# Performance work log

Measured on AMD Instinct MI355X. Metric: run time of the kernel, lower is better.

## Reference

```python
import jax, jax.numpy as jnp
import numpy as np
import itertools

# ---- model dimensions ----
NELEC = 10   # total electrons
NSPIN = 2    # spin_split = 2 -> equal split (5, 5)
NPER = 5     # electrons per spin block
D = 3        # spatial dimension
NION = 2     # number of ions (diatomic)
DP = 32      # backflow output feature dim d'
NDENSE = 64  # ndense_resnet


def _perms_and_signs(n):
    perms = np.array(list(itertools.permutations(range(n))), dtype=np.int32)
    signs = np.empty(len(perms), dtype=np.float32)
    for i, p in enumerate(perms):
        inv = sum(1 for a in range(n) for b in range(a + 1, n) if p[a] > p[b])
        signs[i] = -1.0 if inv % 2 else 1.0
    return jnp.asarray(perms), jnp.asarray(signs)

# constant permutation indices/signs (closed over; not differentiated)
PERMS, SIGNS = _perms_and_signs(NPER)  # (120, 5), (120,)


def setup_inputs() -> dict:
    key = jax.random.key(0)
    ks = jax.random.split(key, 8)
    B = 2048
    feat = NION * D + NION  # backflow input features per electron: r_ei flat + |r_ei|
    nin = NPER * DP         # flattened spin-block input to each ResNet
    return {
        "elec_pos": jax.random.normal(ks[0], (B, NELEC, D), jnp.float32),
        "ion_pos": jax.random.normal(ks[1], (NION, D), jnp.float32) * 2.0,
        "bf_w": jax.random.normal(ks[2], (feat, DP), jnp.float32) / np.sqrt(feat),
        "bf_b": jnp.zeros((DP,), jnp.float32),
        "w0": jax.random.normal(ks[3], (NSPIN, nin, NDENSE), jnp.float32) / np.sqrt(nin),
        "b0": jnp.zeros((NSPIN, NDENSE), jnp.float32),
        "w1": jax.random.normal(ks[4], (NSPIN, NDENSE, NDENSE), jnp.float32) / np.sqrt(NDENSE),
        "b1": jnp.zeros((NSPIN, NDENSE), jnp.float32),
        "w2": jax.random.normal(ks[5], (NSPIN, NDENSE, 1), jnp.float32) / np.sqrt(NDENSE),
        "b2": jnp.zeros((NSPIN, 1), jnp.float32),
        "jastrow_kernel": jnp.ones((NION,), jnp.float32),
    }


def _spin_antisym(block, W0, B0, W1, B1, W2, B2):
    # block: (B, NPER, DP) one spin block of the 1e stream
    B = block.shape[0]
    xp = block[:, PERMS, :]                  # (B, nperm, NPER, DP) all permutations
    xp = xp.reshape(B, PERMS.shape[0], NPER * DP)
    # SimpleResNet: dense->act, residual middle layer, final linear to 1
    h = jnp.tanh(xp @ W0 + B0)
    h = jnp.tanh(h @ W1 + B1) + h            # residual (shapes match)
    out = (h @ W2 + B2)[..., 0]              # (B, nperm)
    return jnp.sum(out * SIGNS, axis=-1)     # signed perm-sum -> (B,)


def reference(elec_pos, ion_pos, bf_w, bf_b, w0, b0, w1, b1, w2, b2, jastrow_kernel):
    B = elec_pos.shape[0]
    # backflow: r_ei features -> dense -> tanh
    r_ei = elec_pos[..., :, None, :] - ion_pos          # (B, nelec, nion, d)
    r_norm = jnp.linalg.norm(r_ei, axis=-1)             # (B, nelec, nion)
    feats = jnp.concatenate([r_ei.reshape(B, NELEC, NION * D), r_norm], axis=-1)
    stream_1e = jnp.tanh(feats @ bf_w + bf_b)           # (B, nelec, DP)
    # split into equal spin blocks (spin_split=2)
    blocks = jnp.stack(jnp.split(stream_1e, NSPIN, axis=-2), axis=0)  # (NSPIN, B, NPER, DP)
    per_spin = jax.vmap(_spin_antisym)(blocks, w0, b0, w1, b1, w2, b2)  # (NSPIN, B)
    antisymmetric_part = jnp.log(jnp.abs(jnp.prod(per_spin, axis=0)))   # (B,)
    # isotropic atomic exponential decay jastrow (log domain)
    jastrow_part = -jnp.sum(jastrow_kernel * r_norm, axis=(-1, -2))     # (B,)
    return antisymmetric_part + jastrow_part
```

## Files before the change

### kernel.cpp

```cpp
#include <hip/hip_runtime.h>
#include <math.h>

#define NELEC 10
#define NSPIN 2
#define NPER 5
#define DIM 3
#define NION 2
#define DP 32
#define NDENSE 64
#define NPERM 120
#define RS 324
#define HTS 124

__device__ __forceinline__ float fast_tanh(float x) {
    float e = __expf(2.0f * x);
    return 1.0f - 2.0f * __builtin_amdgcn_rcpf(e + 1.0f);
}

__device__ __forceinline__ unsigned pick_remove(unsigned& el, int d) {
    unsigned v = (el >> (4 * d)) & 0xFu;
    unsigned low = el & ((1u << (4 * d)) - 1u);
    el = low | ((el >> (4 * (d + 1))) << (4 * d));
    return v;
}

__global__ __launch_bounds__(128, 1) void antisym_kern(
    const float* __restrict__ elec_pos, const float* __restrict__ ion_pos,
    const float* __restrict__ bf_w, const float* __restrict__ bf_b,
    const float* __restrict__ w0, const float* __restrict__ b0,
    const float* __restrict__ w1, const float* __restrict__ b1,
    const float* __restrict__ w2,
    float* __restrict__ psum, int B)
{
    const int b = blockIdx.x;
    const int s = blockIdx.y;
    const int t = threadIdx.x;
    const int wave = t >> 6, lane = t & 63;

    __shared__ float s1e[NPER * DP];
    __shared__ __align__(16) float G[NPER][RS];
    __shared__ __align__(16) float HT[NDENSE][HTS];
    __shared__ double red[4];

    const float* ep = elec_pos + (b * NELEC + s * NPER) * DIM;
    const float i0x = ion_pos[0], i0y = ion_pos[1], i0z = ion_pos[2];
    const float i1x = ion_pos[3], i1y = ion_pos[4], i1z = ion_pos[5];
    for (int idx = t; idx < NPER * DP; idx += 128) {
        int j = idx >> 5, c = idx & 31;
        float ex = ep[j * 3 + 0], ey = ep[j * 3 + 1], ez = ep[j * 3 + 2];
        float dx0 = ex - i0x, dy0 = ey - i0y, dz0 = ez - i0z;
        float dx1 = ex - i1x, dy1 = ey - i1y, dz1 = ez - i1z;
        float n0 = sqrtf(dx0 * dx0 + dy0 * dy0 + dz0 * dz0);
        float n1 = sqrtf(dx1 * dx1 + dy1 * dy1 + dz1 * dz1);
        float acc = bf_b[c];
        acc += dx0 * bf_w[0 * DP + c];
        acc += dy0 * bf_w[1 * DP + c];
        acc += dz0 * bf_w[2 * DP + c];
        acc += dx1 * bf_w[3 * DP + c];
        acc += dy1 * bf_w[4 * DP + c];
        acc += dz1 * bf_w[5 * DP + c];
        acc += n0 * bf_w[6 * DP + c];
        acc += n1 * bf_w[7 * DP + c];
        s1e[idx] = fast_tanh(acc);
    }
    __syncthreads();

    const float* w0s = w0 + s * (NPER * DP) * NDENSE;
    for (int j = wave; j < NPER; j += 2) {
        float4 sv4[8];
        #pragma unroll
        for (int q = 0; q < 8; q++) sv4[q] = *(const float4*)(s1e + j * DP + q * 4);
        #pragma unroll
        for (int i = 0; i < NPER; i++) {
            float acc = 0.f;
            #pragma unroll
            for (int q = 0; q < 8; q++) {
                const float* wb = w0s + (i * DP + q * 4) * NDENSE + lane;
                acc += sv4[q].x * wb[0 * NDENSE];
                acc += sv4[q].y * wb[1 * NDENSE];
                acc += sv4[q].z * wb[2 * NDENSE];
                acc += sv4[q].w * wb[3 * NDENSE];
            }
            G[j][i * NDENSE + lane] = acc;
        }
    }
    __syncthreads();

    const int pid = wave * 60 + lane;
    float sign = 0.f;
    int p0 = 0, p1 = 0, p2 = 0, p3 = 0, p4 = 0;
    if (lane < 60) {
        int p = pid;
        unsigned el = 0x43210u;
        int d0 = p / 24; p -= d0 * 24;
        int d1 = p / 6;  p -= d1 * 6;
        int d2 = p / 2;  p -= d2 * 2;
        int d3 = p;
        p0 = pick_remove(el, d0);
        p1 = pick_remove(el, d1);
        p2 = pick_remove(el, d2);
        p3 = pick_remove(el, d3);
        p4 = el & 0xF;
        sign = ((d0 + d1 + d2 + d3) & 1) ? -1.f : 1.f;
    }

    const float* b0s = b0 + s * NDENSE;
    const float* w2s = w2 + s * NDENSE;
    const float* g0 = &G[p0][0 * NDENSE];
    const float* g1 = &G[p1][1 * NDENSE];
    const float* g2 = &G[p2][2 * NDENSE];
    const float* g3 = &G[p3][3 * NDENSE];
    const float* g4 = &G[p4][4 * NDENSE];

    float hdot = 0.f;
    #pragma unroll
    for (int cc = 0; cc < NDENSE / 4; cc++) {
        float4 a = *(const float4*)(b0s + cc * 4);
        float4 q;
        q = *(const float4*)(g0 + cc * 4); a.x += q.x; a.y += q.y; a.z += q.z; a.w += q.w;
        q = *(const float4*)(g1 + cc * 4); a.x += q.x; a.y += q.y; a.z += q.z; a.w += q.w;
        q = *(const float4*)(g2 + cc * 4); a.x += q.x; a.y += q.y; a.z += q.z; a.w += q.w;
        q = *(const float4*)(g3 + cc * 4); a.x += q.x; a.y += q.y; a.z += q.z; a.w += q.w;
        q = *(const float4*)(g4 + cc * 4); a.x += q.x; a.y += q.y; a.z += q.z; a.w += q.w;
        float t0 = fast_tanh(a.x), t1 = fast_tanh(a.y), t2 = fast_tanh(a.z), t3 = fast_tanh(a.w);
        if (lane < 60) {
            HT[cc * 4 + 0][pid] = t0;
            HT[cc * 4 + 1][pid] = t1;
            HT[cc * 4 + 2][pid] = t2;
            HT[cc * 4 + 3][pid] = t3;
        }
        hdot += t0 * w2s[cc * 4 + 0] + t1 * w2s[cc * 4 + 1]
              + t2 * w2s[cc * 4 + 2] + t3 * w2s[cc * 4 + 3];
    }

    double dvh = (double)(sign * hdot);
    #pragma unroll
    for (int off = 32; off > 0; off >>= 1) dvh += __shfl_down(dvh, off, 64);
    if (lane == 0) red[wave] = dvh;
    __syncthreads();

    const int pg = lane >> 3, jg = lane & 7;
    const int pb = wave ? (56 + 8 * pg) : (8 * pg);
    const float* w1s = w1 + s * NDENSE * NDENSE;
    const float* b1s = b1 + s * NDENSE;
    const float* wgp = w1s + 8 * jg;

    float v[8][8];
    #pragma unroll
    for (int i = 0; i < 8; i++)
        #pragma unroll
        for (int r = 0; r < 8; r++) v[i][r] = 0.f;

    #pragma unroll 4
    for (int k = 0; k < NDENSE; k++) {
        float4 ha = *(const float4*)(&HT[k][pb]);
        float4 hb = *(const float4*)(&HT[k][pb + 4]);
        float4 wa = *(const float4*)(wgp + k * NDENSE);
        float4 wb = *(const float4*)(wgp + k * NDENSE + 4);
        float hv[8] = {ha.x, ha.y, ha.z, ha.w, hb.x, hb.y, hb.z, hb.w};
        float wv[8] = {wa.x, wa.y, wa.z, wa.w, wb.x, wb.y, wb.z, wb.w};
        #pragma unroll
        for (int i = 0; i < 8; i++)
            #pragma unroll
            for (int r = 0; r < 8; r++)
                v[i][r] = fmaf(hv[i], wv[r], v[i][r]);
    }

    float4 b1a = *(const float4*)(b1s + 8 * jg);
    float4 b1b = *(const float4*)(b1s + 8 * jg + 4);
    float4 w2a = *(const float4*)(w2s + 8 * jg);
    float4 w2b = *(const float4*)(w2s + 8 * jg + 4);
    const float b1v[8] = {b1a.x, b1a.y, b1a.z, b1a.w, b1b.x, b1b.y, b1b.z, b1b.w};
    const float w2v[8] = {w2a.x, w2a.y, w2a.z, w2a.w, w2b.x, w2b.y, w2b.z, w2b.w};

    float lanesum = 0.f;
    #pragma unroll
    for (int i = 0; i < 8; i++) {
        int p = pb + i;
        int d0 = p / 24;  int r0 = p - 24 * d0;
        int d1 = r0 / 6;  int r1 = r0 - 6 * d1;
        int d2 = r1 >> 1; int d3 = r1 & 1;
        float sgn = ((d0 + d1 + d2 + d3) & 1) ? -1.f : 1.f;
        if (wave == 1 && pg == 0) sgn = 0.f;
        float si = 0.f;
        #pragma unroll
        for (int r = 0; r < 8; r++)
            si = fmaf(fast_tanh(v[i][r] + b1v[r]), w2v[r], si);
        lanesum = fmaf(sgn, si, lanesum);
    }

    double dvj = (double)lanesum;
    #pragma unroll
    for (int off = 32; off > 0; off >>= 1) dvj += __shfl_down(dvj, off, 64);
    if (lane == 0) red[2 + wave] = dvj;
    __syncthreads();
    if (t == 0) psum[s * B + b] = (float)((red[0] + red[1]) + (red[2] + red[3]));
}

__global__ void combine_kern(const float* __restrict__ psum,
                             const float* __restrict__ elec_pos,
                             const float* __restrict__ ion_pos,
                             const float* __restrict__ jk,
                             float* __restrict__ out, int B)
{
    int b = blockIdx.x * 256 + threadIdx.x;
    if (b >= B) return;
    const float i0x = ion_pos[0], i0y = ion_pos[1], i0z = ion_pos[2];
    const float i1x = ion_pos[3], i1y = ion_pos[4], i1z = ion_pos[5];
    const float j0 = jk[0], j1 = jk[1];
    const float* ep = elec_pos + b * NELEC * DIM;
    float jas = 0.f;
    #pragma unroll
    for (int e = 0; e < NELEC; e++) {
        float ex = ep[e * 3 + 0], ey = ep[e * 3 + 1], ez = ep[e * 3 + 2];
        float dx0 = ex - i0x, dy0 = ey - i0y, dz0 = ez - i0z;
        float dx1 = ex - i1x, dy1 = ey - i1y, dz1 = ez - i1z;
        jas += j0 * sqrtf(dx0 * dx0 + dy0 * dy0 + dz0 * dz0);
        jas += j1 * sqrtf(dx1 * dx1 + dy1 * dy1 + dz1 * dz1);
    }
    float ps0 = psum[b], ps1 = psum[B + b];
    out[b] = logf(fabsf(ps0 * ps1)) - jas;
}

extern "C" void kernel_launch(void* const* d_in, const int* in_sizes, int n_in,
                              void* d_out, int out_size, void* d_ws, size_t ws_size,
                              hipStream_t stream) {
    const float* elec_pos = (const float*)d_in[0];
    const float* ion_pos  = (const float*)d_in[1];
    const float* bf_w     = (const float*)d_in[2];
    const float* bf_b     = (const float*)d_in[3];
    const float* w0       = (const float*)d_in[4];
    const float* b0       = (const float*)d_in[5];
    const float* w1       = (const float*)d_in[6];
    const float* b1       = (const float*)d_in[7];
    const float* w2       = (const float*)d_in[8];
    const float* jk       = (const float*)d_in[10];
    float* out = (float*)d_out;

    const int B = in_sizes[0] / (NELEC * DIM);

    float* psum = (float*)d_ws;

    hipLaunchKernelGGL(antisym_kern,
                       dim3(B, NSPIN), dim3(128), 0, stream,
                       elec_pos, ion_pos, bf_w, bf_b, w0, b0, w1, b1, w2, psum, B);
    hipLaunchKernelGGL(combine_kern,
                       dim3((B + 255) / 256), dim3(256), 0, stream,
                       psum, elec_pos, ion_pos, jk, out, B);
}
```

Before: 165.2 us.

## Double block size to 256 threads and split dense layer work finer

```diff
diff --git a/kernel.cpp b/kernel.cpp
--- a/kernel.cpp
+++ b/kernel.cpp
@@ -24,7 +24,7 @@
     return v;
 }
 
-__global__ __launch_bounds__(128, 1) void antisym_kern(
+__global__ __launch_bounds__(256, 1) void antisym_kern(
     const float* __restrict__ elec_pos, const float* __restrict__ ion_pos,
     const float* __restrict__ bf_w, const float* __restrict__ bf_b,
     const float* __restrict__ w0, const float* __restrict__ b0,
@@ -40,12 +40,13 @@
     __shared__ float s1e[NPER * DP];
     __shared__ __align__(16) float G[NPER][RS];
     __shared__ __align__(16) float HT[NDENSE][HTS];
-    __shared__ double red[4];
+    __shared__ double red_h[2];
+    __shared__ double red_j[4];
 
     const float* ep = elec_pos + (b * NELEC + s * NPER) * DIM;
     const float i0x = ion_pos[0], i0y = ion_pos[1], i0z = ion_pos[2];
     const float i1x = ion_pos[3], i1y = ion_pos[4], i1z = ion_pos[5];
-    for (int idx = t; idx < NPER * DP; idx += 128) {
+    for (int idx = t; idx < NPER * DP; idx += 256) {
         int j = idx >> 5, c = idx & 31;
         float ex = ep[j * 3 + 0], ey = ep[j * 3 + 1], ez = ep[j * 3 + 2];
         float dx0 = ex - i0x, dy0 = ey - i0y, dz0 = ez - i0z;
@@ -66,7 +67,7 @@
     __syncthreads();
 
     const float* w0s = w0 + s * (NPER * DP) * NDENSE;
-    for (int j = wave; j < NPER; j += 2) {
+    for (int j = wave; j < NPER; j += 4) {
         float4 sv4[8];
         #pragma unroll
         for (int q = 0; q < 8; q++) sv4[q] = *(const float4*)(s1e + j * DP + q * 4);
@@ -86,81 +87,82 @@
     }
     __syncthreads();
 
-    const int pid = wave * 60 + lane;
-    float sign = 0.f;
-    int p0 = 0, p1 = 0, p2 = 0, p3 = 0, p4 = 0;
-    if (lane < 60) {
-        int p = pid;
-        unsigned el = 0x43210u;
-        int d0 = p / 24; p -= d0 * 24;
-        int d1 = p / 6;  p -= d1 * 6;
-        int d2 = p / 2;  p -= d2 * 2;
-        int d3 = p;
-        p0 = pick_remove(el, d0);
-        p1 = pick_remove(el, d1);
-        p2 = pick_remove(el, d2);
-        p3 = pick_remove(el, d3);
-        p4 = el & 0xF;
-        sign = ((d0 + d1 + d2 + d3) & 1) ? -1.f : 1.f;
-    }
-
     const float* b0s = b0 + s * NDENSE;
     const float* w2s = w2 + s * NDENSE;
-    const float* g0 = &G[p0][0 * NDENSE];
-    const float* g1 = &G[p1][1 * NDENSE];
-    const float* g2 = &G[p2][2 * NDENSE];
-    const float* g3 = &G[p3][3 * NDENSE];
-    const float* g4 = &G[p4][4 * NDENSE];
-
-    float hdot = 0.f;
-    #pragma unroll
-    for (int cc = 0; cc < NDENSE / 4; cc++) {
-        float4 a = *(const float4*)(b0s + cc * 4);
-        float4 q;
-        q = *(const float4*)(g0 + cc * 4); a.x += q.x; a.y += q.y; a.z += q.z; a.w += q.w;
-        q = *(const float4*)(g1 + cc * 4); a.x += q.x; a.y += q.y; a.z += q.z; a.w += q.w;
-        q = *(const float4*)(g2 + cc * 4); a.x += q.x; a.y += q.y; a.z += q.z; a.w += q.w;
-        q = *(const float4*)(g3 + cc * 4); a.x += q.x; a.y += q.y; a.z += q.z; a.w += q.w;
-        q = *(const float4*)(g4 + cc * 4); a.x += q.x; a.y += q.y; a.z += q.z; a.w += q.w;
-        float t0 = fast_tanh(a.x), t1 = fast_tanh(a.y), t2 = fast_tanh(a.z), t3 = fast_tanh(a.w);
-        if (lane < 60) {
-            HT[cc * 4 + 0][pid] = t0;
-            HT[cc * 4 + 1][pid] = t1;
-            HT[cc * 4 + 2][pid] = t2;
-            HT[cc * 4 + 3][pid] = t3;
+
+    if (wave < 2) {
+        float sign = 0.f;
+        int p0 = 0, p1 = 0, p2 = 0, p3 = 0, p4 = 0;
+        if (t < NPERM) {
+            int p = t;
+            unsigned el = 0x43210u;
+            int d0 = p / 24; p -= d0 * 24;
+            int d1 = p / 6;  p -= d1 * 6;
+            int d2 = p / 2;  p -= d2 * 2;
+            int d3 = p;
+            p0 = pick_remove(el, d0);
+            p1 = pick_remove(el, d1);
+            p2 = pick_remove(el, d2);
+            p3 = pick_remove(el, d3);
+            p4 = el & 0xF;
+            sign = ((d0 + d1 + d2 + d3) & 1) ? -1.f : 1.f;
         }
-        hdot += t0 * w2s[cc * 4 + 0] + t1 * w2s[cc * 4 + 1]
-              + t2 * w2s[cc * 4 + 2] + t3 * w2s[cc * 4 + 3];
-    }
-
-    double dvh = (double)(sign * hdot);
-    #pragma unroll
-    for (int off = 32; off > 0; off >>= 1) dvh += __shfl_down(dvh, off, 64);
-    if (lane == 0) red[wave] = dvh;
-    __syncthreads();
-
-    const int pg = lane >> 3, jg = lane & 7;
-    const int pb = wave ? (56 + 8 * pg) : (8 * pg);
+        const float* g0 = &G[p0][0 * NDENSE];
+        const float* g1 = &G[p1][1 * NDENSE];
+        const float* g2 = &G[p2][2 * NDENSE];
+        const float* g3 = &G[p3][3 * NDENSE];
+        const float* g4 = &G[p4][4 * NDENSE];
+
+        float hdot = 0.f;
+        #pragma unroll
+        for (int cc = 0; cc < NDENSE / 4; cc++) {
+            float4 a = *(const float4*)(b0s + cc * 4);
+            float4 q;
+            q = *(const float4*)(g0 + cc * 4); a.x += q.x; a.y += q.y; a.z += q.z; a.w += q.w;
+            q = *(const float4*)(g1 + cc * 4); a.x += q.x; a.y += q.y; a.z += q.z; a.w += q.w;
+            q = *(const float4*)(g2 + cc * 4); a.x += q.x; a.y += q.y; a.z += q.z; a.w += q.w;
+            q = *(const float4*)(g3 + cc * 4); a.x += q.x; a.y += q.y; a.z += q.z; a.w += q.w;
+            q = *(const float4*)(g4 + cc * 4); a.x += q.x; a.y += q.y; a.z += q.z; a.w += q.w;
+            float t0 = fast_tanh(a.x), t1 = fast_tanh(a.y), t2 = fast_tanh(a.z), t3 = fast_tanh(a.w);
+            if (t < NPERM) {
+                HT[cc * 4 + 0][t] = t0;
+                HT[cc * 4 + 1][t] = t1;
+                HT[cc * 4 + 2][t] = t2;
+                HT[cc * 4 + 3][t] = t3;
+            }
+            hdot += t0 * w2s[cc * 4 + 0] + t1 * w2s[cc * 4 + 1]
+                  + t2 * w2s[cc * 4 + 2] + t3 * w2s[cc * 4 + 3];
+        }
+        double dvh = (double)(sign * hdot);
+        #pragma unroll
+        for (int off = 32; off > 0; off >>= 1) dvh += __shfl_down(dvh, off, 64);
+        if (lane == 0) red_h[wave] = dvh;
+    }
+    __syncthreads();
+
+    const int pg = t >> 3;
+    const int jg = t & 7;
+    const bool pvalid = (pg < 30);
+    const int pb = pvalid ? 4 * pg : 0;
     const float* w1s = w1 + s * NDENSE * NDENSE;
     const float* b1s = b1 + s * NDENSE;
     const float* wgp = w1s + 8 * jg;
 
-    float v[8][8];
-    #pragma unroll
-    for (int i = 0; i < 8; i++)
+    float v[4][8];
+    #pragma unroll
+    for (int i = 0; i < 4; i++)
         #pragma unroll
         for (int r = 0; r < 8; r++) v[i][r] = 0.f;
 
     #pragma unroll 4
     for (int k = 0; k < NDENSE; k++) {
-        float4 ha = *(const float4*)(&HT[k][pb]);
-        float4 hb = *(const float4*)(&HT[k][pb + 4]);
+        float4 hq = *(const float4*)(&HT[k][pb]);
         float4 wa = *(const float4*)(wgp + k * NDENSE);
         float4 wb = *(const float4*)(wgp + k * NDENSE + 4);
-        float hv[8] = {ha.x, ha.y, ha.z, ha.w, hb.x, hb.y, hb.z, hb.w};
-        float wv[8] = {wa.x, wa.y, wa.z, wa.w, wb.x, wb.y, wb.z, wb.w};
-        #pragma unroll
-        for (int i = 0; i < 8; i++)
+        const float hv[4] = {hq.x, hq.y, hq.z, hq.w};
+        const float wv[8] = {wa.x, wa.y, wa.z, wa.w, wb.x, wb.y, wb.z, wb.w};
+        #pragma unroll
+        for (int i = 0; i < 4; i++)
             #pragma unroll
             for (int r = 0; r < 8; r++)
                 v[i][r] = fmaf(hv[i], wv[r], v[i][r]);
@@ -175,13 +177,13 @@
 
     float lanesum = 0.f;
     #pragma unroll
-    for (int i = 0; i < 8; i++) {
+    for (int i = 0; i < 4; i++) {
         int p = pb + i;
         int d0 = p / 24;  int r0 = p - 24 * d0;
         int d1 = r0 / 6;  int r1 = r0 - 6 * d1;
         int d2 = r1 >> 1; int d3 = r1 & 1;
         float sgn = ((d0 + d1 + d2 + d3) & 1) ? -1.f : 1.f;
-        if (wave == 1 && pg == 0) sgn = 0.f;
+        if (!pvalid) sgn = 0.f;
         float si = 0.f;
         #pragma unroll
         for (int r = 0; r < 8; r++)
@@ -192,9 +194,11 @@
     double dvj = (double)lanesum;
     #pragma unroll
     for (int off = 32; off > 0; off >>= 1) dvj += __shfl_down(dvj, off, 64);
-    if (lane == 0) red[2 + wave] = dvj;
-    __syncthreads();
-    if (t == 0) psum[s * B + b] = (float)((red[0] + red[1]) + (red[2] + red[3]));
+    if (lane == 0) red_j[wave] = dvj;
+    __syncthreads();
+    if (t == 0)
+        psum[s * B + b] = (float)((red_h[0] + red_h[1]) +
+                                  ((red_j[0] + red_j[1]) + (red_j[2] + red_j[3])));
 }
 
 __global__ void combine_kern(const float* __restrict__ psum,
@@ -242,7 +246,7 @@
     float* psum = (float*)d_ws;
 
     hipLaunchKernelGGL(antisym_kern,
-                       dim3(B, NSPIN), dim3(128), 0, stream,
+                       dim3(B, NSPIN), dim3(256), 0, stream,
                        elec_pos, ion_pos, bf_w, bf_b, w0, b0, w1, b1, w2, psum, B);
     hipLaunchKernelGGL(combine_kern,
                        dim3((B + 255) / 256), dim3(256), 0, stream,
```

After: 198.3 us. +20.1%, slower.
